# Performance work log

Measured on AMD Instinct MI355X. Metric: run time of the kernel, lower is better.

The kernel has to match this reference:

```python
import jax, jax.numpy as jnp
import numpy as np

B, N, H = 4, 4096, 1024
NH, HD, M = 16, 64, 256
EPS = 1e-5


def gaussian_orthogonal(m, d, rng):
    # scaling=0: rows are orthogonal blocks scaled by norms of fresh gaussian rows
    blocks = []
    n_blocks = (m + d - 1) // d
    for _ in range(n_blocks):
        q, _ = np.linalg.qr(rng.standard_normal((d, d)))
        blocks.append(q.T)
    mat = np.concatenate(blocks, 0)[:m]
    multiplier = np.linalg.norm(rng.standard_normal((m, d)), axis=1)
    return (multiplier[:, None] * mat).astype(np.float32)


def setup_inputs():
    key = jax.random.key(0)
    keys = iter(jax.random.split(key, 24))
    rng = np.random.default_rng(0)

    def w(din, dout):
        return jax.random.normal(next(keys), (din, dout), jnp.float32) * 0.02

    inp = {
        'x': jax.random.normal(next(keys), (B, N, H), jnp.float32),
        'enc_outputs': jax.random.normal(next(keys), (B, N, H), jnp.float32),
    }
    for p in ('sa', 'ca'):
        for q in ('wq', 'wk', 'wv', 'wo'):
            inp[f'{p}_{q}'] = w(H, H)
            inp[f'{p}_b{q[1]}'] = jnp.zeros((H,), jnp.float32)
        inp[f'{p}_proj'] = jnp.asarray(gaussian_orthogonal(M, HD, rng))
    inp['ff_w1'] = w(H, 4 * H); inp['ff_b1'] = jnp.zeros((4 * H,), jnp.float32)
    inp['ff_w2'] = w(4 * H, H); inp['ff_b2'] = jnp.zeros((H,), jnp.float32)
    for i in (1, 2, 3):
        inp[f'ln{i}_g'] = jnp.ones((H,), jnp.float32)
        inp[f'ln{i}_b'] = jnp.zeros((H,), jnp.float32)
    return inp


def _split(t):
    b, n, _ = t.shape
    return t.reshape(b, n, NH, HD).transpose(0, 2, 1, 3)  # [b,h,n,d]


def _feat(data, proj):
    # FAVOR+ nonnegative softmax kernel features
    dn = HD ** -0.25
    dd = jnp.einsum('bhnd,md->bhnm', data * dn, proj)
    diag = 0.5 * (dn ** 2) * jnp.sum(data * data, -1)  # [b,h,n]
    dd = dd - diag[..., None] - jnp.max(dd, axis=-1, keepdims=True)
    return (M ** -0.5) * (jnp.exp(dd) + 1e-4)


def _attn(q, k, v, wq, bq, wk, bk, wv, bv, wo, bo, proj):
    b, n, _ = q.shape
    Q = _split(q @ wq + bq)
    K = _split(k @ wk + bk)
    V = _split(v @ wv + bv)
    Qp = _feat(Q, proj)  # [b,h,n,m]
    Kp = _feat(K, proj)
    denom = jnp.einsum('bhnm,bhm->bhn', Qp, Kp.sum(2))[..., None]
    ctx = jnp.einsum('bhnm,bhnd->bhmd', Kp, V)          # O(N) linear attention
    out = jnp.einsum('bhnm,bhmd->bhnd', Qp, ctx) / denom
    # faithful to torch .view(B,-1,hidden) WITHOUT head transpose-back
    out = out.reshape(b, -1, H)
    return out @ wo + bo


def _ln(x, g, b):
    mu = jnp.mean(x, -1, keepdims=True)
    var = jnp.mean((x - mu) ** 2, -1, keepdims=True)
    return (x - mu) / jnp.sqrt(var + EPS) * g + b


def reference(x, enc_outputs, sa_wq, sa_bq, sa_wk, sa_bk, sa_wv, sa_bv, sa_wo, sa_bo,
              sa_proj, ca_wq, ca_bq, ca_wk, ca_bk, ca_wv, ca_bv, ca_wo, ca_bo, ca_proj,
              ff_w1, ff_b1, ff_w2, ff_b2, ln1_g, ln1_b, ln2_g, ln2_b, ln3_g, ln3_b):
    h = _ln(x + _attn(x, x, x, sa_wq, sa_bq, sa_wk, sa_bk, sa_wv, sa_bv, sa_wo, sa_bo, sa_proj), ln1_g, ln1_b)
    h = _ln(h + _attn(h, enc_outputs, enc_outputs, ca_wq, ca_bq, ca_wk, ca_bk, ca_wv, ca_bv, ca_wo, ca_bo, ca_proj), ln2_g, ln2_b)
    ff = jax.nn.gelu(h @ ff_w1 + ff_b1, approximate=True) @ ff_w2 + ff_b2  # dropout prob 0 -> identity
    return _ln(h + ff, ln3_g, ln3_b)
```

## Files before the change

### kernel.cpp

```cpp
#include <hip/hip_runtime.h>
#include <hip/hip_bf16.h>

#define B_ 4
#define N_ 4096
#define H_ 1024
#define NH_ 16
#define HD_ 64
#define M_ 256

typedef __attribute__((ext_vector_type(8))) __bf16 bf16x8;
typedef __attribute__((ext_vector_type(4))) float f32x4;
typedef __attribute__((ext_vector_type(4))) unsigned int u32x4;

__device__ __forceinline__ float bf2f(unsigned short u) {
  union { unsigned int i; float f; } x; x.i = ((unsigned int)u) << 16; return x.f;
}
__device__ __forceinline__ unsigned short f2b(float f) {
  __hip_bfloat16 h = __float2bfloat16(f);
  return *(unsigned short*)&h;
}
__device__ __forceinline__ float gelu_f(float x) {
  const float c = 0.7978845608028654f;
  float t = tanhf(c * (x + 0.044715f * x * x * x));
  return 0.5f * x * (1.0f + t);
}
__device__ __forceinline__ bf16x8 ones8() {
  union { unsigned int u[4]; bf16x8 v; } o;
  o.u[0] = 0x3F803F80u; o.u[1] = 0x3F803F80u; o.u[2] = 0x3F803F80u; o.u[3] = 0x3F803F80u;
  return o.v;
}

typedef __attribute__((address_space(3))) unsigned int as3_uint;
typedef const __attribute__((address_space(1))) unsigned int as1_uint;
__device__ __forceinline__ void gload16(const void* g, void* l) {
  __builtin_amdgcn_global_load_lds((as1_uint*)g, (as3_uint*)l, 16, 0, 0);
}

template<int ACT>
__launch_bounds__(256)
__global__ void gemm_mfma(const unsigned short* __restrict__ A, int lda,
                          const unsigned short* __restrict__ BT,
                          const float* __restrict__ bias,
                          unsigned short* __restrict__ C, int ldc, int K) {
  __shared__ __align__(16) char LDS[65536];

  const int tid = threadIdx.x;
  const int nwg = gridDim.x * gridDim.y;
  const int lin = blockIdx.y * gridDim.x + blockIdx.x;
  const int mm = (lin & 7) * (nwg >> 3) + (lin >> 3);
  const int bx = mm % gridDim.x, by = mm / gridDim.x;
  const int row0 = by * 128;
  const int col0 = bx * 128;

  const int w = tid >> 6, lane = tid & 63;
  const int wm = w >> 1, wn = w & 1;
  const int ln = lane & 15, hi = lane >> 4;
  const int rswz = (ln & 7) << 4;

  const int srow = w * 8 + (lane >> 3);
  const int schunk = ((lane & 7) ^ (lane >> 3)) * 8;
  const unsigned short* Ag = A + (long long)(row0 + srow) * lda + schunk;
  const unsigned short* Bg = BT + (long long)(col0 + srow) * K + schunk;
  const int ldsw = w * 1024;

  f32x4 acc[4][4];
#pragma unroll
  for (int i = 0; i < 4; ++i)
#pragma unroll
    for (int j = 0; j < 4; ++j) acc[i][j] = (f32x4){0.f, 0.f, 0.f, 0.f};

  auto STAGE = [&](int p, int k0) {
    char* dst = LDS + p * 32768 + ldsw;
#pragma unroll
    for (int i = 0; i < 4; ++i) {
      gload16(Ag + (long long)i * 32 * lda + k0, dst + i * 4096);
      gload16(Bg + (long long)i * 32 * K + k0, dst + 16384 + i * 4096);
    }
  };
  auto COMPUTE = [&](int p) {
    char* AsB = LDS + p * 32768;
    char* BsB = AsB + 16384;
#pragma unroll
    for (int kc = 0; kc < 2; ++kc) {
      const int koff = (kc * 64 + hi * 16) ^ rswz;
      bf16x8 av[4], bv[4];
#pragma unroll
      for (int i = 0; i < 4; ++i)
        av[i] = *(bf16x8*)(AsB + (wm * 64 + i * 16 + ln) * 128 + koff);
#pragma unroll
      for (int j = 0; j < 4; ++j)
        bv[j] = *(bf16x8*)(BsB + (wn * 64 + j * 16 + ln) * 128 + koff);
      __builtin_amdgcn_s_setprio(1);
#pragma unroll
      for (int i = 0; i < 4; ++i)
#pragma unroll
        for (int j = 0; j < 4; ++j)
          acc[i][j] = __builtin_amdgcn_mfma_f32_16x16x32_bf16(av[i], bv[j], acc[i][j], 0, 0, 0);
      __builtin_amdgcn_s_setprio(0);
    }
  };

  STAGE(0, 0);
  __syncthreads();
  int cur = 0;
  for (int k0 = 64; k0 < K; k0 += 64) {
    STAGE(cur ^ 1, k0);
    COMPUTE(cur);
    __syncthreads();
    cur ^= 1;
  }
  COMPUTE(cur);
  __syncthreads();

  char* SB = LDS;
#pragma unroll
  for (int j = 0; j < 4; ++j) {
    const int lcol = wn * 64 + j * 16 + ln;
    const float bj = bias ? bias[col0 + lcol] : 0.0f;
#pragma unroll
    for (int i = 0; i < 4; ++i) {
      const int rb_ = wm * 64 + i * 16 + hi * 4;
#pragma unroll
      for (int r = 0; r < 4; ++r) {
        float v = acc[i][j][r] + bj;
        if (ACT == 1) v = gelu_f(v);
        const int row = rb_ + r;
        *(unsigned short*)(SB + ((row * 256 + lcol * 2) ^ ((row & 7) << 4))) = f2b(v);
      }
    }
  }
  __syncthreads();
#pragma unroll
  for (int p = 0; p < 8; ++p) {
    const int idx = p * 256 + tid;
    const int row = idx >> 4, seg = idx & 15;
    u32x4 v = *(u32x4*)(SB + ((row * 256 + seg * 16) ^ ((row & 7) << 4)));
    __builtin_nontemporal_store(v, (u32x4*)(C + (long long)(row0 + row) * ldc + col0 + seg * 8));
  }
}

__launch_bounds__(256)
__global__ void ctxksum_mfma(const unsigned short* __restrict__ QKV,
                             const unsigned short* __restrict__ pjB,
                             float* __restrict__ ksumP,
                             float* __restrict__ ctxP) {
  __shared__ char Kt[8192];
  __shared__ char Vt[8192];
  __shared__ char Pt[32768];
  __shared__ float rmaxL[4][64];
  __shared__ float ssqL[64];
  const int z = blockIdx.z, b = z >> 4, hh = z & 15;
  const int sp = blockIdx.x;
  const long long n0 = sp * 512;
  const unsigned short* Kg = QKV + (long long)(b * 4096) * 3072 + 1024 + hh * 64;
  const unsigned short* Vg = QKV + (long long)(b * 4096) * 3072 + 2048 + hh * 64;
  const int tid = threadIdx.x;
  const int w = tid >> 6, lane = tid & 63;
  const int ln = lane & 15, hi = lane >> 4;
  const int rswz = (ln & 7) << 4;
  const bf16x8 onesf = ones8();

  f32x4 accC[4][4];
#pragma unroll
  for (int i = 0; i < 4; ++i)
#pragma unroll
    for (int j = 0; j < 4; ++j) accC[i][j] = (f32x4){0.f, 0.f, 0.f, 0.f};
  f32x4 accK[4];
#pragma unroll
  for (int i = 0; i < 4; ++i) accK[i] = (f32x4){0.f, 0.f, 0.f, 0.f};

  for (int t = 0; t < 8; ++t) {
    const long long nt = n0 + t * 64;
    __syncthreads();
#pragma unroll
    for (int p = 0; p < 2; ++p) {
      int id = p * 256 + tid;
      int r = id >> 3, c = id & 7;
      gload16(Kg + (nt + r) * 3072 + ((c ^ (r & 7)) * 8), Kt + id * 16);
    }
    {
      int n = tid >> 2, d0 = (tid & 3) * 16;
      const unsigned short* src = Vg + (nt + n) * 3072 + d0;
      ushort4 v0 = *(const ushort4*)src;
      ushort4 v1 = *(const ushort4*)(src + 4);
      ushort4 v2 = *(const ushort4*)(src + 8);
      ushort4 v3 = *(const ushort4*)(src + 12);
      unsigned short vals[16] = {v0.x, v0.y, v0.z, v0.w, v1.x, v1.y, v1.z, v1.w,
                                 v2.x, v2.y, v2.z, v2.w, v3.x, v3.y, v3.z, v3.w};
#pragma unroll
      for (int e = 0; e < 16; ++e) {
        int d = d0 + e;
        *(unsigned short*)(Vt + ((d * 128 + n * 2) ^ ((d & 7) << 4))) = vals[e];
      }
    }
    __syncthreads();

    f32x4 accT[4][4];
#pragma unroll
    for (int i = 0; i < 4; ++i)
#pragma unroll
      for (int j = 0; j < 4; ++j) accT[i][j] = (f32x4){0.f, 0.f, 0.f, 0.f};
#pragma unroll
    for (int kc = 0; kc < 2; ++kc) {
      const int koff = (kc * 64 + hi * 16) ^ rswz;
      bf16x8 kv[4], bq[4];
#pragma unroll
      for (int nj = 0; nj < 4; ++nj)
        kv[nj] = *(bf16x8*)(Kt + (nj * 16 + ln) * 128 + koff);
#pragma unroll
      for (int mi = 0; mi < 4; ++mi)
        bq[mi] = *(const bf16x8*)(pjB + (w * 64 + mi * 16 + ln) * 64 + kc * 32 + hi * 8);
      __builtin_amdgcn_s_setprio(1);
#pragma unroll
      for (int mi = 0; mi < 4; ++mi)
#pragma unroll
        for (int nj = 0; nj < 4; ++nj)
          accT[mi][nj] = __builtin_amdgcn_mfma_f32_16x16x32_bf16(bq[mi], kv[nj], accT[mi][nj], 0, 0, 0);
      __builtin_amdgcn_s_setprio(0);
    }

#pragma unroll
    for (int nj = 0; nj < 4; ++nj) {
      float mx = accT[0][nj][0];
#pragma unroll
      for (int mi = 0; mi < 4; ++mi)
#pragma unroll
        for (int r = 0; r < 4; ++r) mx = fmaxf(mx, accT[mi][nj][r]);
      mx = fmaxf(mx, __shfl_xor(mx, 16, 64));
      mx = fmaxf(mx, __shfl_xor(mx, 32, 64));
      if (hi == 0) rmaxL[w][nj * 16 + ln] = mx;
    }
    {
      int r = tid >> 2, q = tid & 3;
      int b0 = (r * 128 + q * 32) ^ ((r & 7) << 4);
      int b1 = (r * 128 + q * 32 + 16) ^ ((r & 7) << 4);
      u32x4 x0 = *(u32x4*)(Kt + b0);
      u32x4 x1 = *(u32x4*)(Kt + b1);
      float s = 0.f;
#pragma unroll
      for (int e = 0; e < 4; ++e) {
        float a0 = bf2f((unsigned short)(x0[e] & 0xffff)), a1 = bf2f((unsigned short)(x0[e] >> 16));
        float a2 = bf2f((unsigned short)(x1[e] & 0xffff)), a3 = bf2f((unsigned short)(x1[e] >> 16));
        s += a0 * a0 + a1 * a1 + a2 * a2 + a3 * a3;
      }
      s += __shfl_xor(s, 1, 64);
      s += __shfl_xor(s, 2, 64);
      if (q == 0) ssqL[r] = s;
    }
    __syncthreads();

    float base[4];
#pragma unroll
    for (int nj = 0; nj < 4; ++nj) {
      int n = nj * 16 + ln;
      base[nj] = 0.0625f * ssqL[n] +
                 fmaxf(fmaxf(rmaxL[0][n], rmaxL[1][n]), fmaxf(rmaxL[2][n], rmaxL[3][n]));
    }
#pragma unroll
    for (int mi = 0; mi < 4; ++mi)
#pragma unroll
      for (int nj = 0; nj < 4; ++nj)
#pragma unroll
        for (int r = 0; r < 4; ++r) {
          float v = 0.0625f * (expf(accT[mi][nj][r] - base[nj]) + 1e-4f);
          int m = w * 64 + mi * 16 + hi * 4 + r;
          int n = nj * 16 + ln;
          *(unsigned short*)(Pt + ((m * 128 + n * 2) ^ ((m & 7) << 4))) = f2b(v);
        }
    __syncthreads();

#pragma unroll
    for (int kc = 0; kc < 2; ++kc) {
      const int koff = (kc * 64 + hi * 16) ^ rswz;
      bf16x8 am[4], bv[4];
#pragma unroll
      for (int i = 0; i < 4; ++i)
        am[i] = *(bf16x8*)(Pt + (w * 64 + i * 16 + ln) * 128 + koff);
#pragma unroll
      for (int j = 0; j < 4; ++j)
        bv[j] = *(bf16x8*)(Vt + (j * 16 + ln) * 128 + koff);
      __builtin_amdgcn_s_setprio(1);
#pragma unroll
      for (int i = 0; i < 4; ++i)
#pragma unroll
        for (int j = 0; j < 4; ++j)
          accC[i][j] = __builtin_amdgcn_mfma_f32_16x16x32_bf16(am[i], bv[j], accC[i][j], 0, 0, 0);
#pragma unroll
      for (int i = 0; i < 4; ++i)
        accK[i] = __builtin_amdgcn_mfma_f32_16x16x32_bf16(am[i], onesf, accK[i], 0, 0, 0);
      __builtin_amdgcn_s_setprio(0);
    }
  }

  if (ln == 0) {
#pragma unroll
    for (int mi = 0; mi < 4; ++mi)
#pragma unroll
      for (int r = 0; r < 4; ++r)
        ksumP[((long long)z * 8 + sp) * 256 + w * 64 + mi * 16 + hi * 4 + r] = accK[mi][r];
  }

  float* ctxPs = ctxP + ((long long)z * 8 + sp) * 16384;
#pragma unroll
  for (int dh = 0; dh < 2; ++dh) {
    __syncthreads();
#pragma unroll
    for (int i = 0; i < 4; ++i)
#pragma unroll
      for (int jj = 0; jj < 2; ++jj) {
        int j = dh * 2 + jj;
#pragma unroll
        for (int r = 0; r < 4; ++r) {
          int m = w * 64 + i * 16 + hi * 4 + r;
          int dl = jj * 16 + ln;
          *(float*)(Pt + ((m * 128 + dl * 4) ^ ((m & 7) << 4))) = accC[i][j][r];
        }
      }
    __syncthreads();
#pragma unroll
    for (int p = 0; p < 8; ++p) {
      int idx = p * 256 + tid;
      int row = idx >> 3, seg = idx & 7;
      u32x4 v = *(u32x4*)(Pt + ((row * 128 + seg * 16) ^ ((row & 7) << 4)));
      __builtin_nontemporal_store(v, (u32x4*)(ctxPs + dh * 8192 + row * 32 + seg * 4));
    }
  }
}

__launch_bounds__(256)
__global__ void ctx_fin(const float* __restrict__ ctxP, const float* __restrict__ ksumP,
                        unsigned short* __restrict__ ctxbf, float* __restrict__ ksumF) {
  __shared__ float acc[16384];
  const int z = blockIdx.x;
  const int tid = threadIdx.x;
  const float* base = ctxP + (long long)z * 8 * 16384;
  for (int i = tid; i < 16384; i += 256) {
    float s = 0.f;
#pragma unroll
    for (int q = 0; q < 8; ++q) s += base[(long long)q * 16384 + i];
    acc[i] = s;
  }
  {
    const float* kb = ksumP + (long long)z * 8 * 256;
    float s = 0.f;
#pragma unroll
    for (int q = 0; q < 8; ++q) s += kb[q * 256 + tid];
    ksumF[z * 256 + tid] = s;
  }
  __syncthreads();
  unsigned short* dst = ctxbf + (long long)z * 16384;
  for (int cc = tid; cc < 2048; cc += 256) {
    int mh = cc >> 10, rem = cc & 1023, d = rem >> 4, cl = rem & 15;
    int m0 = mh * 128 + cl * 8;
    int dh = d >> 5, dl = d & 31;
    ushort4 o0, o1;
    o0.x = f2b(acc[dh * 8192 + (m0 + 0) * 32 + dl]);
    o0.y = f2b(acc[dh * 8192 + (m0 + 1) * 32 + dl]);
    o0.z = f2b(acc[dh * 8192 + (m0 + 2) * 32 + dl]);
    o0.w = f2b(acc[dh * 8192 + (m0 + 3) * 32 + dl]);
    o1.x = f2b(acc[dh * 8192 + (m0 + 4) * 32 + dl]);
    o1.y = f2b(acc[dh * 8192 + (m0 + 5) * 32 + dl]);
    o1.z = f2b(acc[dh * 8192 + (m0 + 6) * 32 + dl]);
    o1.w = f2b(acc[dh * 8192 + (m0 + 7) * 32 + dl]);
    unsigned short* p = dst + (long long)mh * 8192 + (d * 16 + (cl ^ (d & 7))) * 8;
    *(ushort4*)p = o0;
    *(ushort4*)(p + 4) = o1;
  }
}

__launch_bounds__(256)
__global__ void ao_fused(const unsigned short* __restrict__ QKV,
                         const unsigned short* __restrict__ pjB,
                         const float* __restrict__ ksum,
                         const unsigned short* __restrict__ ctxbf,
                         unsigned short* __restrict__ AO) {
  __shared__ char Qt[8192];
  __shared__ char Ps[32768];
  __shared__ char Ch[32768];
  __shared__ float rmaxL[4][64];
  __shared__ float ssqL[64];
  __shared__ float dprt[4][64];
  __shared__ float denomS[64];
  __shared__ float ksL[256];
  const int z = blockIdx.z, b = z >> 4, hh = z & 15;
  const int n0 = blockIdx.x * 64;
  const unsigned short* Qg = QKV + (long long)(b * 4096) * 3072 + hh * 64;
  const int tid = threadIdx.x;
  const int w = tid >> 6, lane = tid & 63;
  const int ln = lane & 15, hi = lane >> 4;
  const int rswz = (ln & 7) << 4;

#pragma unroll
  for (int p = 0; p < 8; ++p) {
    int id = p * 256 + tid;
    gload16(ctxbf + (long long)z * 16384 + id * 8, Ch + id * 16);
  }
#pragma unroll
  for (int p = 0; p < 2; ++p) {
    int id = p * 256 + tid;
    int r = id >> 3, c = id & 7;
    gload16(Qg + (long long)(n0 + r) * 3072 + ((c ^ (r & 7)) * 8), Qt + id * 16);
  }
  ksL[tid] = ksum[z * 256 + tid];
  __syncthreads();

  f32x4 accT[4][4];
#pragma unroll
  for (int i = 0; i < 4; ++i)
#pragma unroll
    for (int j = 0; j < 4; ++j) accT[i][j] = (f32x4){0.f, 0.f, 0.f, 0.f};
#pragma unroll
  for (int kc = 0; kc < 2; ++kc) {
    const int koff = (kc * 64 + hi * 16) ^ rswz;
    bf16x8 qv[4], bq[4];
#pragma unroll
    for (int nj = 0; nj < 4; ++nj)
      qv[nj] = *(bf16x8*)(Qt + (nj * 16 + ln) * 128 + koff);
#pragma unroll
    for (int mi = 0; mi < 4; ++mi)
      bq[mi] = *(const bf16x8*)(pjB + (w * 64 + mi * 16 + ln) * 64 + kc * 32 + hi * 8);
    __builtin_amdgcn_s_setprio(1);
#pragma unroll
    for (int mi = 0; mi < 4; ++mi)
#pragma unroll
      for (int nj = 0; nj < 4; ++nj)
        accT[mi][nj] = __builtin_amdgcn_mfma_f32_16x16x32_bf16(bq[mi], qv[nj], accT[mi][nj], 0, 0, 0);
    __builtin_amdgcn_s_setprio(0);
  }

#pragma unroll
  for (int nj = 0; nj < 4; ++nj) {
    float mx = accT[0][nj][0];
#pragma unroll
    for (int mi = 0; mi < 4; ++mi)
#pragma unroll
      for (int r = 0; r < 4; ++r) mx = fmaxf(mx, accT[mi][nj][r]);
    mx = fmaxf(mx, __shfl_xor(mx, 16, 64));
    mx = fmaxf(mx, __shfl_xor(mx, 32, 64));
    if (hi == 0) rmaxL[w][nj * 16 + ln] = mx;
  }
  {
    int r = tid >> 2, q = tid & 3;
    int b0 = (r * 128 + q * 32) ^ ((r & 7) << 4);
    int b1 = (r * 128 + q * 32 + 16) ^ ((r & 7) << 4);
    u32x4 x0 = *(u32x4*)(Qt + b0);
    u32x4 x1 = *(u32x4*)(Qt + b1);
    float s = 0.f;
#pragma unroll
    for (int e = 0; e < 4; ++e) {
      float a0 = bf2f((unsigned short)(x0[e] & 0xffff)), a1 = bf2f((unsigned short)(x0[e] >> 16));
      float a2 = bf2f((unsigned short)(x1[e] & 0xffff)), a3 = bf2f((unsigned short)(x1[e] >> 16));
      s += a0 * a0 + a1 * a1 + a2 * a2 + a3 * a3;
    }
    s += __shfl_xor(s, 1, 64);
    s += __shfl_xor(s, 2, 64);
    if (q == 0) ssqL[r] = s;
  }
  __syncthreads();

  float base[4];
#pragma unroll
  for (int nj = 0; nj < 4; ++nj) {
    int n = nj * 16 + ln;
    base[nj] = 0.0625f * ssqL[n] +
               fmaxf(fmaxf(rmaxL[0][n], rmaxL[1][n]), fmaxf(rmaxL[2][n], rmaxL[3][n]));
  }
  float ksv[4][4];
#pragma unroll
  for (int mi = 0; mi < 4; ++mi)
#pragma unroll
    for (int r = 0; r < 4; ++r)
      ksv[mi][r] = ksL[w * 64 + mi * 16 + hi * 4 + r];
  float dp[4] = {0.f, 0.f, 0.f, 0.f};
#pragma unroll
  for (int mi = 0; mi < 4; ++mi)
#pragma unroll
    for (int nj = 0; nj < 4; ++nj)
#pragma unroll
      for (int r = 0; r < 4; ++r) {
        float v = 0.0625f * (expf(accT[mi][nj][r] - base[nj]) + 1e-4f);
        unsigned short vb = f2b(v);
        int m = w * 64 + mi * 16 + hi * 4 + r;
        int n = nj * 16 + ln;
        *(unsigned short*)(Ps + n * 512 + ((m * 2) ^ ((n & 7) << 4))) = vb;
        dp[nj] += bf2f(vb) * ksv[mi][r];
      }
#pragma unroll
  for (int nj = 0; nj < 4; ++nj) {
    dp[nj] += __shfl_xor(dp[nj], 16, 64);
    dp[nj] += __shfl_xor(dp[nj], 32, 64);
    if (hi == 0) dprt[w][nj * 16 + ln] = dp[nj];
  }
  __syncthreads();
  if (tid < 64) denomS[tid] = dprt[0][tid] + dprt[1][tid] + dprt[2][tid] + dprt[3][tid];

  f32x4 accO[4];
#pragma unroll
  for (int j = 0; j < 4; ++j) accO[j] = (f32x4){0.f, 0.f, 0.f, 0.f};
#pragma unroll
  for (int mh = 0; mh < 2; ++mh) {
#pragma unroll
    for (int ms = 0; ms < 4; ++ms) {
      const int koff = (ms * 64 + hi * 16);
      bf16x8 ap = *(bf16x8*)(Ps + (w * 16 + ln) * 512 + ((mh * 256 + koff) ^ rswz));
      bf16x8 bc[4];
#pragma unroll
      for (int j = 0; j < 4; ++j)
        bc[j] = *(bf16x8*)(Ch + mh * 16384 + (j * 16 + ln) * 256 + (koff ^ rswz));
      __builtin_amdgcn_s_setprio(1);
#pragma unroll
      for (int j = 0; j < 4; ++j)
        accO[j] = __builtin_amdgcn_mfma_f32_16x16x32_bf16(ap, bc[j], accO[j], 0, 0, 0);
      __builtin_amdgcn_s_setprio(0);
    }
  }
  __syncthreads();

  float inv[4];
#pragma unroll
  for (int r = 0; r < 4; ++r) inv[r] = 1.0f / denomS[w * 16 + hi * 4 + r];
  char* Ct = Qt;
#pragma unroll
  for (int j = 0; j < 4; ++j)
#pragma unroll
    for (int r = 0; r < 4; ++r) {
      int n = w * 16 + hi * 4 + r;
      int d = j * 16 + ln;
      *(unsigned short*)(Ct + ((n * 128 + d * 2) ^ ((n & 7) << 4))) = f2b(accO[j][r] * inv[r]);
    }
  __syncthreads();
#pragma unroll
  for (int p = 0; p < 2; ++p) {
    int idx = p * 256 + tid;
    int row = idx >> 3, seg = idx & 7;
    u32x4 v = *(u32x4*)(Ct + ((row * 128 + seg * 16) ^ ((row & 7) << 4)));
    *(u32x4*)(AO + (long long)(b * 4096 + n0 + row) * 1024 + hh * 64 + seg * 8) = v;
  }
}

__launch_bounds__(256)
__global__ void wt_cvt(const float* __restrict__ in, unsigned short* __restrict__ out,
                       int K, int N) {
  __shared__ float t[32][33];
  int k0 = blockIdx.y * 32, n0 = blockIdx.x * 32;
  int tx = threadIdx.x & 31, ty = threadIdx.x >> 5;
  for (int r = ty; r < 32; r += 8) t[r][tx] = in[(long long)(k0 + r) * N + n0 + tx];
  __syncthreads();
  for (int r = ty; r < 32; r += 8) out[(long long)(n0 + r) * K + k0 + tx] = f2b(t[tx][r]);
}

__launch_bounds__(256)
__global__ void projB_cvt(const float* __restrict__ proj, unsigned short* __restrict__ out) {
  int i = blockIdx.x * 256 + threadIdx.x;
  out[i] = f2b(0.35355339059327373f * proj[i]);
}

__launch_bounds__(256)
__global__ void bias_cat(const float* __restrict__ b0, const float* __restrict__ b1,
                         const float* __restrict__ b2, float* __restrict__ out) {
  int i = blockIdx.x * 256 + threadIdx.x;
  float v;
  if (i < 1024) v = b0[i];
  else if (i < 2048) v = b1[i - 1024];
  else v = b2[i - 2048];
  out[i] = v;
}

__launch_bounds__(256)
__global__ void cvt_bf16(const float* __restrict__ in, unsigned short* __restrict__ out,
                         long long n) {
  long long stride = (long long)gridDim.x * 1024;
  for (long long i = ((long long)blockIdx.x * 256 + threadIdx.x) * 4; i < n; i += stride) {
    float4 v = *(const float4*)&in[i];
    ushort4 o;
    o.x = f2b(v.x); o.y = f2b(v.y); o.z = f2b(v.z); o.w = f2b(v.w);
    *(ushort4*)&out[i] = o;
  }
}

__launch_bounds__(256)
__global__ void ln_k(const float* __restrict__ resf, const unsigned short* __restrict__ resb,
                     const unsigned short* __restrict__ po,
                     const float* __restrict__ g, const float* __restrict__ be,
                     float* __restrict__ outf, unsigned short* __restrict__ outb) {
  long long row = blockIdx.x;
  int t = threadIdx.x;
  float x0, x1, x2, x3;
  if (resf) {
    float4 va = ((const float4*)(resf + row * H_))[t];
    x0 = va.x; x1 = va.y; x2 = va.z; x3 = va.w;
  } else {
    ushort4 va = ((const ushort4*)(resb + row * H_))[t];
    x0 = bf2f(va.x); x1 = bf2f(va.y); x2 = bf2f(va.z); x3 = bf2f(va.w);
  }
  {
    ushort4 vp = ((const ushort4*)(po + row * H_))[t];
    x0 += bf2f(vp.x); x1 += bf2f(vp.y); x2 += bf2f(vp.z); x3 += bf2f(vp.w);
  }
  float s = x0 + x1 + x2 + x3;
  float q = x0 * x0 + x1 * x1 + x2 * x2 + x3 * x3;
#pragma unroll
  for (int m = 1; m < 64; m <<= 1) { s += __shfl_xor(s, m, 64); q += __shfl_xor(q, m, 64); }
  __shared__ float ssum[4], ssq[4];
  int w = t >> 6, lane = t & 63;
  if (lane == 0) { ssum[w] = s; ssq[w] = q; }
  __syncthreads();
  s = ssum[0] + ssum[1] + ssum[2] + ssum[3];
  q = ssq[0] + ssq[1] + ssq[2] + ssq[3];
  float mean = s * (1.0f / H_);
  float var = q * (1.0f / H_) - mean * mean;
  float rstd = rsqrtf(var + 1e-5f);
  float4 vg = ((const float4*)g)[t];
  float4 vbe = ((const float4*)be)[t];
  float o0 = (x0 - mean) * rstd * vg.x + vbe.x;
  float o1 = (x1 - mean) * rstd * vg.y + vbe.y;
  float o2 = (x2 - mean) * rstd * vg.z + vbe.z;
  float o3 = (x3 - mean) * rstd * vg.w + vbe.w;
  if (outf) {
    float4 o; o.x = o0; o.y = o1; o.z = o2; o.w = o3;
    ((float4*)(outf + row * H_))[t] = o;
  }
  if (outb) {
    ushort4 ob; ob.x = f2b(o0); ob.y = f2b(o1); ob.z = f2b(o2); ob.w = f2b(o3);
    ((ushort4*)(outb + row * H_))[t] = ob;
  }
}

extern "C" void kernel_launch(void* const* d_in, const int* in_sizes, int n_in,
                              void* d_out, int out_size, void* d_ws, size_t ws_size,
                              hipStream_t stream) {
  (void)in_sizes; (void)n_in; (void)out_size; (void)ws_size;
  const float* x      = (const float*)d_in[0];
  const float* enc    = (const float*)d_in[1];
  const float* sa_w[4] = {(const float*)d_in[2], (const float*)d_in[4], (const float*)d_in[6], (const float*)d_in[8]};
  const float* sa_b[4] = {(const float*)d_in[3], (const float*)d_in[5], (const float*)d_in[7], (const float*)d_in[9]};
  const float* sa_pj  = (const float*)d_in[10];
  const float* ca_w[4] = {(const float*)d_in[11], (const float*)d_in[13], (const float*)d_in[15], (const float*)d_in[17]};
  const float* ca_b[4] = {(const float*)d_in[12], (const float*)d_in[14], (const float*)d_in[16], (const float*)d_in[18]};
  const float* ca_pj  = (const float*)d_in[19];
  const float* ff_w1  = (const float*)d_in[20];
  const float* ff_b1  = (const float*)d_in[21];
  const float* ff_w2  = (const float*)d_in[22];
  const float* ff_b2  = (const float*)d_in[23];
  const float* ln1_g  = (const float*)d_in[24];
  const float* ln1_b  = (const float*)d_in[25];
  const float* ln2_g  = (const float*)d_in[26];
  const float* ln2_b  = (const float*)d_in[27];
  const float* ln3_g  = (const float*)d_in[28];
  const float* ln3_b  = (const float*)d_in[29];

  float* ws = (float*)d_ws;
  unsigned short* XB = (unsigned short*)(ws);
  unsigned short* EB = (unsigned short*)(ws + 8388608LL);
  unsigned short* QKVb = (unsigned short*)(ws + 16777216LL);
  unsigned short* PO = (unsigned short*)(ws + 41943040LL);
  float* ctxP = ws + 41943040LL;
  unsigned short* MIDB = PO;
  unsigned short* FO = (unsigned short*)(ws + 50331648LL);
  unsigned short* WTph = (unsigned short*)(ws + 52428800LL);
  unsigned short* pjB = (unsigned short*)(ws + 54525952LL);
  float* ksumP = ws + 54542336LL;
  float* ksumF = ws + 54673408LL;
  unsigned short* ctxbf = (unsigned short*)(ws + 55607296LL);
  float* biasC = ws + 56131584LL;

  unsigned short* ff1T = EB;
  unsigned short* ff2T = EB + 4194304LL;
  unsigned short* pjB_sa = pjB, *pjB_ca = pjB + 16384;

  dim3 blk(256, 1, 1);
  const int LDQ = 3072;

  projB_cvt<<<dim3(64), blk, 0, stream>>>(sa_pj, pjB_sa);
  projB_cvt<<<dim3(64), blk, 0, stream>>>(ca_pj, pjB_ca);
  cvt_bf16<<<dim3(2048), blk, 0, stream>>>(x, XB, 16777216LL);

  auto attn_core = [&](const unsigned short* pj, const float* wo_bias) {
    ctxksum_mfma<<<dim3(8, 1, 64), blk, 0, stream>>>(QKVb, pj, ksumP, ctxP);
    ctx_fin<<<dim3(64), blk, 0, stream>>>(ctxP, ksumP, ctxbf, ksumF);
    ao_fused<<<dim3(64, 1, 64), blk, 0, stream>>>(QKVb, pj, ksumF, ctxbf, EB);
    gemm_mfma<0><<<dim3(8, 128), blk, 0, stream>>>(EB, H_, WTph + 3145728, wo_bias, PO, H_, H_);
  };

  for (int i = 0; i < 4; ++i)
    wt_cvt<<<dim3(32, 32), blk, 0, stream>>>(sa_w[i], WTph + (long long)i * 1048576, H_, H_);
  bias_cat<<<dim3(12), blk, 0, stream>>>(sa_b[0], sa_b[1], sa_b[2], biasC);
  gemm_mfma<0><<<dim3(24, 128), blk, 0, stream>>>(XB, H_, WTph, biasC, QKVb, LDQ, H_);
  attn_core(pjB_sa, sa_b[3]);
  ln_k<<<dim3(16384), blk, 0, stream>>>(x, nullptr, PO, ln1_g, ln1_b, nullptr, XB);

  cvt_bf16<<<dim3(2048), blk, 0, stream>>>(enc, EB, 16777216LL);
  for (int i = 0; i < 4; ++i)
    wt_cvt<<<dim3(32, 32), blk, 0, stream>>>(ca_w[i], WTph + (long long)i * 1048576, H_, H_);
  bias_cat<<<dim3(8), blk, 0, stream>>>(ca_b[1], ca_b[2], nullptr, biasC);
  gemm_mfma<0><<<dim3(8, 128), blk, 0, stream>>>(XB, H_, WTph, ca_b[0], QKVb, LDQ, H_);
  gemm_mfma<0><<<dim3(16, 128), blk, 0, stream>>>(EB, H_, WTph + 1048576, biasC, QKVb + 1024, LDQ, H_);
  attn_core(pjB_ca, ca_b[3]);
  ln_k<<<dim3(16384), blk, 0, stream>>>(nullptr, XB, PO, ln2_g, ln2_b, nullptr, XB);

  wt_cvt<<<dim3(128, 32), blk, 0, stream>>>(ff_w1, ff1T, H_, 4096);
  wt_cvt<<<dim3(32, 128), blk, 0, stream>>>(ff_w2, ff2T, 4096, H_);
  for (int c = 0; c < 4; ++c) {
    const long long co = (long long)c * 4096 * H_;
    gemm_mfma<1><<<dim3(32, 32), blk, 0, stream>>>(XB + co, H_, ff1T, ff_b1, MIDB, 4096, H_);
    gemm_mfma<0><<<dim3(8, 32), blk, 0, stream>>>(MIDB, 4096, ff2T, ff_b2, FO, H_, 4096);
    ln_k<<<dim3(4096), blk, 0, stream>>>(nullptr, XB + co, FO, ln3_g, ln3_b,
                                         (float*)d_out + co, nullptr);
  }
}
```

Baseline: 1.358 ms.

## Double-buffer K/V tiles in ctxksum, batch weight conversions, halve FFN chunks

The ctxksum kernel now double-buffers its K and V shared-memory tiles. The next tile's K async load and V register load are issued before the current tile's feature computation, which overlaps global latency with MFMA work and removes one barrier per iteration. The four per-weight transpose launches and the two projection conversions are each merged into a single launch. The FFN now runs in two chunks of 8192 rows instead of four, reusing the QKV and PO buffers as larger scratch space, so there are fewer launches and bigger grids. The cost is higher LDS use in ctxksum, which may lower occupancy, and a dependence on buffer-aliasing assumptions.

```diff
diff --git a/kernel.cpp b/kernel.cpp
--- a/kernel.cpp
+++ b/kernel.cpp
@@ -144,8 +144,8 @@
                              const unsigned short* __restrict__ pjB,
                              float* __restrict__ ksumP,
                              float* __restrict__ ctxP) {
-  __shared__ char Kt[8192];
-  __shared__ char Vt[8192];
+  __shared__ char Kt[2][8192];
+  __shared__ char Vt[2][8192];
   __shared__ char Pt[32768];
   __shared__ float rmaxL[4][64];
   __shared__ float ssqL[64];
@@ -169,31 +169,46 @@
 #pragma unroll
   for (int i = 0; i < 4; ++i) accK[i] = (f32x4){0.f, 0.f, 0.f, 0.f};
 
-  for (int t = 0; t < 8; ++t) {
-    const long long nt = n0 + t * 64;
-    __syncthreads();
+  const int vn = tid >> 2, vd0 = (tid & 3) * 16;
+  ushort4 vr[4];
+  auto VLOAD = [&](long long nt) {
+    const unsigned short* src = Vg + (nt + vn) * 3072 + vd0;
+    vr[0] = *(const ushort4*)src;
+    vr[1] = *(const ushort4*)(src + 4);
+    vr[2] = *(const ushort4*)(src + 8);
+    vr[3] = *(const ushort4*)(src + 12);
+  };
+  auto VWRITE = [&](int buf) {
+    unsigned short vals[16] = {vr[0].x, vr[0].y, vr[0].z, vr[0].w,
+                               vr[1].x, vr[1].y, vr[1].z, vr[1].w,
+                               vr[2].x, vr[2].y, vr[2].z, vr[2].w,
+                               vr[3].x, vr[3].y, vr[3].z, vr[3].w};
+#pragma unroll
+    for (int e = 0; e < 16; ++e) {
+      int d = vd0 + e;
+      *(unsigned short*)(Vt[buf] + ((d * 128 + vn * 2) ^ ((d & 7) << 4))) = vals[e];
+    }
+  };
+  auto KSTAGE = [&](long long nt, int buf) {
 #pragma unroll
     for (int p = 0; p < 2; ++p) {
       int id = p * 256 + tid;
       int r = id >> 3, c = id & 7;
-      gload16(Kg + (nt + r) * 3072 + ((c ^ (r & 7)) * 8), Kt + id * 16);
-    }
-    {
-      int n = tid >> 2, d0 = (tid & 3) * 16;
-      const unsigned short* src = Vg + (nt + n) * 3072 + d0;
-      ushort4 v0 = *(const ushort4*)src;
-      ushort4 v1 = *(const ushort4*)(src + 4);
-      ushort4 v2 = *(const ushort4*)(src + 8);
-      ushort4 v3 = *(const ushort4*)(src + 12);
-      unsigned short vals[16] = {v0.x, v0.y, v0.z, v0.w, v1.x, v1.y, v1.z, v1.w,
-                                 v2.x, v2.y, v2.z, v2.w, v3.x, v3.y, v3.z, v3.w};
-#pragma unroll
-      for (int e = 0; e < 16; ++e) {
-        int d = d0 + e;
-        *(unsigned short*)(Vt + ((d * 128 + n * 2) ^ ((d & 7) << 4))) = vals[e];
-      }
-    }
-    __syncthreads();
+      gload16(Kg + (nt + r) * 3072 + ((c ^ (r & 7)) * 8), Kt[buf] + id * 16);
+    }
+  };
+
+  KSTAGE(n0, 0);
+  VLOAD(n0);
+  VWRITE(0);
+  __syncthreads();
+
+  for (int t = 0; t < 8; ++t) {
+    const int cur = t & 1;
+    if (t < 7) {
+      KSTAGE(n0 + (t + 1) * 64, cur ^ 1);
+      VLOAD(n0 + (t + 1) * 64);
+    }
 
     f32x4 accT[4][4];
 #pragma unroll
@@ -206,7 +221,7 @@
       bf16x8 kv[4], bq[4];
 #pragma unroll
       for (int nj = 0; nj < 4; ++nj)
-        kv[nj] = *(bf16x8*)(Kt + (nj * 16 + ln) * 128 + koff);
+        kv[nj] = *(bf16x8*)(Kt[cur] + (nj * 16 + ln) * 128 + koff);
 #pragma unroll
       for (int mi = 0; mi < 4; ++mi)
         bq[mi] = *(const bf16x8*)(pjB + (w * 64 + mi * 16 + ln) * 64 + kc * 32 + hi * 8);
@@ -234,8 +249,8 @@
       int r = tid >> 2, q = tid & 3;
       int b0 = (r * 128 + q * 32) ^ ((r & 7) << 4);
       int b1 = (r * 128 + q * 32 + 16) ^ ((r & 7) << 4);
-      u32x4 x0 = *(u32x4*)(Kt + b0);
-      u32x4 x1 = *(u32x4*)(Kt + b1);
+      u32x4 x0 = *(u32x4*)(Kt[cur] + b0);
+      u32x4 x1 = *(u32x4*)(Kt[cur] + b1);
       float s = 0.f;
 #pragma unroll
       for (int e = 0; e < 4; ++e) {
@@ -267,6 +282,7 @@
           int n = nj * 16 + ln;
           *(unsigned short*)(Pt + ((m * 128 + n * 2) ^ ((m & 7) << 4))) = f2b(v);
         }
+    if (t < 7) VWRITE(cur ^ 1);
     __syncthreads();
 
 #pragma unroll
@@ -278,7 +294,7 @@
         am[i] = *(bf16x8*)(Pt + (w * 64 + i * 16 + ln) * 128 + koff);
 #pragma unroll
       for (int j = 0; j < 4; ++j)
-        bv[j] = *(bf16x8*)(Vt + (j * 16 + ln) * 128 + koff);
+        bv[j] = *(bf16x8*)(Vt[cur] + (j * 16 + ln) * 128 + koff);
       __builtin_amdgcn_s_setprio(1);
 #pragma unroll
       for (int i = 0; i < 4; ++i)
@@ -550,9 +566,26 @@
 }
 
 __launch_bounds__(256)
-__global__ void projB_cvt(const float* __restrict__ proj, unsigned short* __restrict__ out) {
+__global__ void wt_cvt4(const float* __restrict__ w0, const float* __restrict__ w1,
+                        const float* __restrict__ w2, const float* __restrict__ w3,
+                        unsigned short* __restrict__ out) {
+  __shared__ float t[32][33];
+  const float* in = (blockIdx.z == 0) ? w0 : (blockIdx.z == 1) ? w1
+                    : (blockIdx.z == 2) ? w2 : w3;
+  unsigned short* o = out + (long long)blockIdx.z * 1048576;
+  int k0 = blockIdx.y * 32, n0 = blockIdx.x * 32;
+  int tx = threadIdx.x & 31, ty = threadIdx.x >> 5;
+  for (int r = ty; r < 32; r += 8) t[r][tx] = in[(long long)(k0 + r) * H_ + n0 + tx];
+  __syncthreads();
+  for (int r = ty; r < 32; r += 8) o[(long long)(n0 + r) * H_ + k0 + tx] = f2b(t[tx][r]);
+}
+
+__launch_bounds__(256)
+__global__ void projB_cvt2(const float* __restrict__ pj_sa, const float* __restrict__ pj_ca,
+                           unsigned short* __restrict__ out) {
   int i = blockIdx.x * 256 + threadIdx.x;
-  out[i] = f2b(0.35355339059327373f * proj[i]);
+  const float* src = (i < 16384) ? pj_sa : pj_ca;
+  out[i] = f2b(0.35355339059327373f * src[i & 16383]);
 }
 
 __launch_bounds__(256)
@@ -655,8 +688,8 @@
   unsigned short* QKVb = (unsigned short*)(ws + 16777216LL);
   unsigned short* PO = (unsigned short*)(ws + 41943040LL);
   float* ctxP = ws + 41943040LL;
-  unsigned short* MIDB = PO;
-  unsigned short* FO = (unsigned short*)(ws + 50331648LL);
+  unsigned short* MID2 = QKVb;
+  unsigned short* FO2 = PO;
   unsigned short* WTph = (unsigned short*)(ws + 52428800LL);
   unsigned short* pjB = (unsigned short*)(ws + 54525952LL);
   float* ksumP = ws + 54542336LL;
@@ -671,8 +704,7 @@
   dim3 blk(256, 1, 1);
   const int LDQ = 3072;
 
-  projB_cvt<<<dim3(64), blk, 0, stream>>>(sa_pj, pjB_sa);
-  projB_cvt<<<dim3(64), blk, 0, stream>>>(ca_pj, pjB_ca);
+  projB_cvt2<<<dim3(128), blk, 0, stream>>>(sa_pj, ca_pj, pjB);
   cvt_bf16<<<dim3(2048), blk, 0, stream>>>(x, XB, 16777216LL);
 
   auto attn_core = [&](const unsigned short* pj, const float* wo_bias) {
@@ -682,16 +714,14 @@
     gemm_mfma<0><<<dim3(8, 128), blk, 0, stream>>>(EB, H_, WTph + 3145728, wo_bias, PO, H_, H_);
   };
 
-  for (int i = 0; i < 4; ++i)
-    wt_cvt<<<dim3(32, 32), blk, 0, stream>>>(sa_w[i], WTph + (long long)i * 1048576, H_, H_);
+  wt_cvt4<<<dim3(32, 32, 4), blk, 0, stream>>>(sa_w[0], sa_w[1], sa_w[2], sa_w[3], WTph);
   bias_cat<<<dim3(12), blk, 0, stream>>>(sa_b[0], sa_b[1], sa_b[2], biasC);
   gemm_mfma<0><<<dim3(24, 128), blk, 0, stream>>>(XB, H_, WTph, biasC, QKVb, LDQ, H_);
   attn_core(pjB_sa, sa_b[3]);
   ln_k<<<dim3(16384), blk, 0, stream>>>(x, nullptr, PO, ln1_g, ln1_b, nullptr, XB);
 
   cvt_bf16<<<dim3(2048), blk, 0, stream>>>(enc, EB, 16777216LL);
-  for (int i = 0; i < 4; ++i)
-    wt_cvt<<<dim3(32, 32), blk, 0, stream>>>(ca_w[i], WTph + (long long)i * 1048576, H_, H_);
+  wt_cvt4<<<dim3(32, 32, 4), blk, 0, stream>>>(ca_w[0], ca_w[1], ca_w[2], ca_w[3], WTph);
   bias_cat<<<dim3(8), blk, 0, stream>>>(ca_b[1], ca_b[2], nullptr, biasC);
   gemm_mfma<0><<<dim3(8, 128), blk, 0, stream>>>(XB, H_, WTph, ca_b[0], QKVb, LDQ, H_);
   gemm_mfma<0><<<dim3(16, 128), blk, 0, stream>>>(EB, H_, WTph + 1048576, biasC, QKVb + 1024, LDQ, H_);
@@ -700,11 +730,11 @@
 
   wt_cvt<<<dim3(128, 32), blk, 0, stream>>>(ff_w1, ff1T, H_, 4096);
   wt_cvt<<<dim3(32, 128), blk, 0, stream>>>(ff_w2, ff2T, 4096, H_);
-  for (int c = 0; c < 4; ++c) {
-    const long long co = (long long)c * 4096 * H_;
-    gemm_mfma<1><<<dim3(32, 32), blk, 0, stream>>>(XB + co, H_, ff1T, ff_b1, MIDB, 4096, H_);
-    gemm_mfma<0><<<dim3(8, 32), blk, 0, stream>>>(MIDB, 4096, ff2T, ff_b2, FO, H_, 4096);
-    ln_k<<<dim3(4096), blk, 0, stream>>>(nullptr, XB + co, FO, ln3_g, ln3_b,
+  for (int c = 0; c < 2; ++c) {
+    const long long co = (long long)c * 8192 * H_;
+    gemm_mfma<1><<<dim3(32, 64), blk, 0, stream>>>(XB + co, H_, ff1T, ff_b1, MID2, 4096, H_);
+    gemm_mfma<0><<<dim3(8, 64), blk, 0, stream>>>(MID2, 4096, ff2T, ff_b2, FO2, H_, 4096);
+    ln_k<<<dim3(8192), blk, 0, stream>>>(nullptr, XB + co, FO2, ln3_g, ln3_b,
                                          (float*)d_out + co, nullptr);
   }
 }
```

Result: faster. 1.243 ms (-8.4%).
